# Kernel tuning notes

Hardware: AMD Instinct MI355X
Metric: run time of the kernel (lower is better)

## Reference

```python
import jax, jax.numpy as jnp
import numpy as np

B, N, C = 16, 2048, 256  # dim=256, hidden_dim=2*dim -> v,gate each width C
LN_EPS = 1e-5


def setup_inputs() -> dict:
    key = jax.random.key(0)
    ks = jax.random.split(key, 6)
    std = 0.02
    return {
        "x": jax.random.normal(ks[0], (B, N, C), dtype=jnp.float32),
        "H": 64,
        "W": 32,
        "ln_w": jnp.ones((C,), jnp.float32),
        "ln_b": jnp.zeros((C,), jnp.float32),
        "w_hidden": jax.random.normal(ks[1], (C, 2 * C), jnp.float32) * std,
        "b_hidden": jnp.zeros((2 * C,), jnp.float32),
        "w_kv": jax.random.normal(ks[2], (C, C), jnp.float32) * std,  # qkv_bias=False
        "gamma": jnp.ones((2, C), jnp.float32),   # torch.ones(2, dim)
        "beta": jnp.zeros((2, C), jnp.float32),   # torch.zeros(2, dim)
        "w_proj": jax.random.normal(ks[3], (C, C), jnp.float32) * std,
        "b_proj": jnp.zeros((C,), jnp.float32),
    }


def reference(x, H, W, ln_w, ln_b, w_hidden, b_hidden, w_kv, gamma, beta, w_proj, b_proj):
    # H, W are unused by the original forward (pos conv is dead code).
    b, n, c = x.shape
    # LayerNorm
    mu = jnp.mean(x, axis=-1, keepdims=True)
    var = jnp.mean(jnp.square(x - mu), axis=-1, keepdims=True)
    normed = (x - mu) * jax.lax.rsqrt(var + LN_EPS) * ln_w + ln_b
    # to_hidden: Linear + SiLU, then chunk into v, gate (each width c)
    h = jax.nn.silu(normed @ w_hidden + b_hidden)
    v, gate = h[..., :c], h[..., c:]
    # kv projection, then offset-scale into q, k
    Z = normed @ w_kv                                  # (b, n, c)
    QK = Z[..., None, :] * gamma + beta                # (b, n, 2, c)
    q, k = QK[..., 0, :], QK[..., 1, :]
    # relu^2 quadratic attention (no softmax)
    attn = jnp.einsum('bid,bjd->bij', q, k) / n        # (b, n, n)
    A = jnp.square(jax.nn.relu(attn))
    V = jnp.einsum('bij,bjd->bid', A, v)               # (b, n, c)
    # SiLU gating, output projection, residual
    out = (V * gate) @ w_proj + b_proj
    return out + x
```

## Files before the change

kernel.cpp:

```cpp
#include <hip/hip_runtime.h>

#define BN 32768
#define NB 16
#define NN 2048
#define CC 256
#define JT 64
#define NTILES (NN / JT)

using short8  = __attribute__((ext_vector_type(8))) short;
using floatx4 = __attribute__((ext_vector_type(4))) float;

__device__ __forceinline__ unsigned short f2bf(float f) {
  unsigned u = __builtin_bit_cast(unsigned, f);
  u += 0x7fffu + ((u >> 16) & 1u);
  return (unsigned short)(u >> 16);
}
__device__ __forceinline__ float bf2f(unsigned short h) {
  unsigned u = ((unsigned)h) << 16;
  return __builtin_bit_cast(float, u);
}
__device__ __forceinline__ unsigned pk4fp8(float a, float b, float c, float d) {
  unsigned u = __builtin_amdgcn_cvt_pk_fp8_f32(c, d, 0, true);
  return __builtin_amdgcn_cvt_pk_fp8_f32(a, b, (int)u, false);
}
__device__ __forceinline__ long lo64(uint4 v) {
  uint2 t; t.x = v.x; t.y = v.y; return __builtin_bit_cast(long, t);
}
__device__ __forceinline__ long hi64(uint4 v) {
  uint2 t; t.x = v.z; t.y = v.w; return __builtin_bit_cast(long, t);
}
__device__ __forceinline__ void gll16(const void* g, void* l) {
  __builtin_amdgcn_global_load_lds(
      (const __attribute__((address_space(1))) void*)g,
      (__attribute__((address_space(3))) void*)l, 16, 0, 0);
}

__global__ __launch_bounds__(256) void ln_kernel(
    const float* __restrict__ x, const float* __restrict__ lw,
    const float* __restrict__ lb, unsigned short* __restrict__ normed) {
  int row  = blockIdx.x * 4 + (threadIdx.x >> 6);
  int lane = threadIdx.x & 63;
  float4 v = ((const float4*)(x + (size_t)row * CC))[lane];
  float s  = v.x + v.y + v.z + v.w;
  float s2 = v.x * v.x + v.y * v.y + v.z * v.z + v.w * v.w;
#pragma unroll
  for (int off = 32; off; off >>= 1) {
    s  += __shfl_xor(s, off);
    s2 += __shfl_xor(s2, off);
  }
  float mu = s * (1.0f / CC);
  float rs = rsqrtf(s2 * (1.0f / CC) - mu * mu + 1e-5f);
  float4 w = ((const float4*)lw)[lane];
  float4 b = ((const float4*)lb)[lane];
  ushort4 o;
  o.x = f2bf((v.x - mu) * rs * w.x + b.x);
  o.y = f2bf((v.y - mu) * rs * w.y + b.y);
  o.z = f2bf((v.z - mu) * rs * w.z + b.z);
  o.w = f2bf((v.w - mu) * rs * w.w + b.w);
  ((ushort4*)(normed + (size_t)row * CC))[lane] = o;
}

__global__ __launch_bounds__(256) void wconv_kernel(
    const float* __restrict__ wh, const float* __restrict__ wkv,
    const float* __restrict__ wp,
    unsigned short* __restrict__ wTh, unsigned short* __restrict__ wTkv,
    unsigned short* __restrict__ wTp) {
  __shared__ float T[64][65];
  int bid = blockIdx.x;
  const float* src; unsigned short* dst; int N, kt, nt;
  if (bid < 32)      { src = wh;  dst = wTh;  N = 512; kt = bid >> 3;        nt = bid & 7; }
  else if (bid < 48) { src = wkv; dst = wTkv; N = 256; kt = (bid - 32) >> 2; nt = (bid - 32) & 3; }
  else               { src = wp;  dst = wTp;  N = 256; kt = (bid - 48) >> 2; nt = (bid - 48) & 3; }
  int k0 = kt * 64, n0 = nt * 64;
  int t = threadIdx.x;
  int r = t >> 2, c0 = (t & 3) * 16;
#pragma unroll
  for (int e = 0; e < 4; ++e)
    *(float4*)(&T[r][c0 + e * 4]) =
        *(const float4*)(src + (size_t)(k0 + r) * N + n0 + c0 + e * 4);
  __syncthreads();
#pragma unroll
  for (int e = 0; e < 16; ++e)
    dst[(size_t)(n0 + r) * 256 + k0 + c0 + e] = f2bf(T[c0 + e][r]);
}

__global__ __launch_bounds__(256) void gemm_v(
    const unsigned short* __restrict__ A, const unsigned short* __restrict__ BT,
    const float* __restrict__ bias, unsigned char* __restrict__ vB) {
  __shared__ unsigned char img[16384];
  int wave = threadIdx.x >> 6, lane = threadIdx.x & 63;
  int m = lane & 15, g4 = lane >> 4, kb = g4 * 8;
  int mb = blockIdx.x * 128;
  int nq = blockIdx.y * 128;
  int m0 = mb + (wave & 1) * 64;
  int n0 = nq + (wave >> 1) * 64;
  floatx4 acc[4][4] = {};
#pragma unroll
  for (int ks = 0; ks < 8; ++ks) {
    short8 af[4], bf[4];
#pragma unroll
    for (int i = 0; i < 4; ++i)
      af[i] = *(const short8*)(A + (size_t)(m0 + i * 16 + m) * CC + ks * 32 + kb);
#pragma unroll
    for (int j = 0; j < 4; ++j)
      bf[j] = *(const short8*)(BT + (size_t)(n0 + j * 16 + m) * CC + ks * 32 + kb);
#pragma unroll
    for (int i = 0; i < 4; ++i)
#pragma unroll
      for (int j = 0; j < 4; ++j)
        acc[i][j] = __builtin_amdgcn_mfma_f32_16x16x32_bf16(af[i], bf[j], acc[i][j], 0, 0, 0);
  }
  const int sw = (m >> 1) & 3;
  const int jtl = (wave & 1);
  const int jp4 = (g4 & 1) * 4;
  const int g4h = g4 >> 1;
#pragma unroll
  for (int j = 0; j < 4; ++j) {
    int col = n0 + j * 16 + m;
    int cl = col - nq;
    float bv = bias[col];
#pragma unroll
    for (int i = 0; i < 4; ++i) {
      int g4a = ((i * 2 + g4h) & 3) ^ sw;
      int h8 = ((i >> 1) & 1) * 8;
      float h, s0, s1, s2, s3;
      h = acc[i][j][0] + bv; s0 = h / (1.0f + __expf(-h));
      h = acc[i][j][1] + bv; s1 = h / (1.0f + __expf(-h));
      h = acc[i][j][2] + bv; s2 = h / (1.0f + __expf(-h));
      h = acc[i][j][3] + bv; s3 = h / (1.0f + __expf(-h));
      *(unsigned*)(img + jtl * 8192 + cl * 64 + g4a * 16 + h8 + jp4) =
          pk4fp8(s0, s1, s2, s3);
    }
  }
  __syncthreads();
  const size_t tb = ((size_t)(mb >> 11) * 32 + ((mb & 2047) >> 6)) * 16384;
#pragma unroll
  for (int it = 0; it < 4; ++it) {
    int o = it * 4096 + threadIdx.x * 16;
    int jl = o >> 13, rem = o & 8191;
    *(uint4*)(vB + tb + (size_t)jl * 16384 + (size_t)nq * 64 + rem) =
        *(const uint4*)(img + o);
  }
}

__global__ __launch_bounds__(256) void gemm_gate(
    const unsigned short* __restrict__ A, const unsigned short* __restrict__ BT,
    const float* __restrict__ bias, unsigned short* __restrict__ gout) {
  int wave = threadIdx.x >> 6, lane = threadIdx.x & 63;
  int m = lane & 15, g4 = lane >> 4, kb = g4 * 8;
  int m0 = blockIdx.x * 128 + (wave & 1) * 64;
  int n0 = 256 + blockIdx.y * 128 + (wave >> 1) * 64;
  floatx4 acc[4][4] = {};
#pragma unroll
  for (int ks = 0; ks < 8; ++ks) {
    short8 af[4], bf[4];
#pragma unroll
    for (int i = 0; i < 4; ++i)
      af[i] = *(const short8*)(A + (size_t)(m0 + i * 16 + m) * CC + ks * 32 + kb);
#pragma unroll
    for (int j = 0; j < 4; ++j)
      bf[j] = *(const short8*)(BT + (size_t)(n0 + j * 16 + m) * CC + ks * 32 + kb);
#pragma unroll
    for (int i = 0; i < 4; ++i)
#pragma unroll
      for (int j = 0; j < 4; ++j)
        acc[i][j] = __builtin_amdgcn_mfma_f32_16x16x32_bf16(af[i], bf[j], acc[i][j], 0, 0, 0);
  }
#pragma unroll
  for (int j = 0; j < 4; ++j) {
    int col = n0 + j * 16 + m;
    float bv = bias[col];
#pragma unroll
    for (int i = 0; i < 4; ++i)
#pragma unroll
      for (int r = 0; r < 4; ++r) {
        int row = m0 + i * 16 + g4 * 4 + r;
        float hh = acc[i][j][r] + bv;
        float sv = hh / (1.0f + __expf(-hh));
        gout[(size_t)row * CC + col - 256] = f2bf(sv);
      }
  }
}

__global__ __launch_bounds__(256) void gemm_kv(
    const unsigned short* __restrict__ A, const unsigned short* __restrict__ BT,
    const float* __restrict__ gamma, const float* __restrict__ beta,
    unsigned char* __restrict__ qout, unsigned char* __restrict__ kout) {
  __shared__ unsigned char kvimg[32768];
  int wave = threadIdx.x >> 6, lane = threadIdx.x & 63;
  int m = lane & 15, g4 = lane >> 4, kb = g4 * 8;
  int m0 = blockIdx.x * 128 + (wave & 1) * 64;
  int n0 = blockIdx.y * 128 + (wave >> 1) * 64;
  floatx4 acc[4][4] = {};
#pragma unroll
  for (int ks = 0; ks < 8; ++ks) {
    short8 af[4], bf[4];
#pragma unroll
    for (int i = 0; i < 4; ++i)
      af[i] = *(const short8*)(A + (size_t)(m0 + i * 16 + m) * CC + ks * 32 + kb);
#pragma unroll
    for (int j = 0; j < 4; ++j)
      bf[j] = *(const short8*)(BT + (size_t)(n0 + j * 16 + m) * CC + ks * 32 + kb);
#pragma unroll
    for (int i = 0; i < 4; ++i)
#pragma unroll
      for (int j = 0; j < 4; ++j)
        acc[i][j] = __builtin_amdgcn_mfma_f32_16x16x32_bf16(bf[j], af[i], acc[i][j], 0, 0, 0);
  }
  const int sw = (m >> 1) & 3;
  unsigned char* qi = kvimg;
  unsigned char* ki = kvimg + 16384;
  const int jbw = (wave & 1) * 4;
  const int ksl = (wave >> 1);
#pragma unroll
  for (int j = 0; j < 4; ++j) {
    int c4 = n0 + j * 16 + g4 * 4;
    float4 g0 = *(const float4*)(gamma + c4);
    float4 b0 = *(const float4*)(beta + c4);
    float4 g1 = *(const float4*)(gamma + CC + c4);
    float4 b1 = *(const float4*)(beta + CC + c4);
    int slot = ((c4 >> 3) & 3) ^ sw;
    int sub = slot * 16 + ((c4 >> 5) & 1) * 8 + (c4 & 7);
    int lbase = ksl * 1024 + m * 64 + sub;
#pragma unroll
    for (int i = 0; i < 4; ++i) {
      int off = (jbw + i) * 2048 + lbase;
      floatx4 z = acc[i][j];
      *(unsigned*)(qi + off) = pk4fp8(z[0] * g0.x + b0.x, z[1] * g0.y + b0.y,
                                      z[2] * g0.z + b0.z, z[3] * g0.w + b0.w);
      *(unsigned*)(ki + off) = pk4fp8(z[0] * g1.x + b1.x, z[1] * g1.y + b1.y,
                                      z[2] * g1.z + b1.z, z[3] * g1.w + b1.w);
    }
  }
  __syncthreads();
  const int mb = blockIdx.x * 128;
  const int jg0 = (mb & 2047) >> 4;
  const int kg0 = blockIdx.y * 2;
  const size_t gbase = ((size_t)(mb >> 11) * 128 + jg0) * 4096;
#pragma unroll
  for (int it = 0; it < 4; ++it) {
    int o = it * 4096 + threadIdx.x * 16;
    int jbl = o >> 11, rem = o & 2047;
    int ks2l = rem >> 10, r2 = rem & 1023;
    size_t gaddr = gbase + (size_t)jbl * 4096 + (size_t)(kg0 + ks2l) * 1024 + r2;
    *(uint4*)(kout + gaddr) = *(const uint4*)(ki + o);
    int n15 = (r2 >> 6) & 15;
    int slot = (r2 >> 4) & 3;
    int os = (o & ~48) | (((slot ^ ((n15 >> 1) & 3)) & 3) << 4);
    *(uint4*)(qout + gaddr) = *(const uint4*)(qi + os);
  }
}

__global__ __launch_bounds__(256, 2) void attn_kernel(
    const unsigned char* __restrict__ qB, const unsigned char* __restrict__ kB,
    const unsigned char* __restrict__ vB, const unsigned short* __restrict__ gg,
    unsigned short* __restrict__ og) {
  __shared__ unsigned char Kl[2][16384];
  __shared__ unsigned char Vl[2][16384];
  const int tid = threadIdx.x;
  const int wave = tid >> 6, lane = tid & 63;
  const int m = lane & 15, g4 = lane >> 4;
  const int id = blockIdx.x;
  const int b = id & 15, bx = id >> 4;
  const int i0 = bx * 64;
  const unsigned char* kimg = kB + (size_t)b * 524288;
  const unsigned char* vimg = vB + (size_t)b * 524288;

  const int iblk = bx * 4 + wave;
  uint4 qf[4];
#pragma unroll
  for (int ks2 = 0; ks2 < 4; ++ks2)
    qf[ks2] = *(const uint4*)(qB + ((size_t)(b * 128 + iblk) * 4 + ks2) * 1024 + m * 64 + g4 * 16);

  floatx4 acc[16] = {};
  const int alo = (m + ((g4 & 1) << 5)) << 2;
  const int ahi = alo + 64;
  const int gsw = (g4 ^ ((m >> 1) & 3)) * 16;

  auto stage = [&](int buf, int t) {
    const unsigned char* kt = kimg + (size_t)t * 16384;
    const unsigned char* vt = vimg + (size_t)t * 16384;
#pragma unroll
    for (int it = 0; it < 4; ++it) {
      int o = (it * 256 + tid) * 16;
      gll16(kt + o, &Kl[buf][o]);
      gll16(vt + o, &Vl[buf][o]);
    }
  };

  stage(0, 0);
  for (int t = 0; t < NTILES; ++t) {
    const int cur = t & 1;
    __syncthreads();
    if (t + 1 < NTILES) stage(cur ^ 1, t + 1);
    floatx4 sacc[4] = {};
#pragma unroll
    for (int ks2 = 0; ks2 < 4; ++ks2) {
#pragma unroll
      for (int jf = 0; jf < 4; ++jf) {
        uint4 kf = *(const uint4*)(&Kl[cur][(jf * 4 + ks2) * 1024 + m * 64 + gsw]);
        sacc[jf] = __builtin_amdgcn_mfma_f32_16x16x32_fp8_fp8(
            lo64(kf), lo64(qf[ks2]), sacc[jf], 0, 0, 0);
        sacc[jf] = __builtin_amdgcn_mfma_f32_16x16x32_fp8_fp8(
            hi64(kf), hi64(qf[ks2]), sacc[jf], 0, 0, 0);
      }
    }
    unsigned pk[4];
#pragma unroll
    for (int jf = 0; jf < 4; ++jf) {
      float p0 = fmaxf(sacc[jf][0], 0.0f) * 0.0625f;
      float p1 = fmaxf(sacc[jf][1], 0.0f) * 0.0625f;
      float p2 = fmaxf(sacc[jf][2], 0.0f) * 0.0625f;
      float p3 = fmaxf(sacc[jf][3], 0.0f) * 0.0625f;
      pk[jf] = pk4fp8(p0 * p0, p1 * p1, p2 * p2, p3 * p3);
    }
    long ap[2];
#pragma unroll
    for (int kk = 0; kk < 2; ++kk) {
      int A0 = __builtin_amdgcn_ds_bpermute(alo, (int)pk[2 * kk]);
      int B0 = __builtin_amdgcn_ds_bpermute(alo, (int)pk[2 * kk + 1]);
      int C0 = __builtin_amdgcn_ds_bpermute(ahi, (int)pk[2 * kk]);
      int D0 = __builtin_amdgcn_ds_bpermute(ahi, (int)pk[2 * kk + 1]);
      unsigned lo = (g4 & 2) ? (unsigned)B0 : (unsigned)A0;
      unsigned hi = (g4 & 2) ? (unsigned)D0 : (unsigned)C0;
      ap[kk] = (long)(((unsigned long long)hi << 32) | lo);
    }
#pragma unroll
    for (int cf = 0; cf < 16; ++cf) {
      uint4 vfr = *(const uint4*)(&Vl[cur][cf * 1024 + m * 64 + gsw]);
      acc[cf] = __builtin_amdgcn_mfma_f32_16x16x32_fp8_fp8(ap[0], lo64(vfr), acc[cf], 0, 0, 0);
      acc[cf] = __builtin_amdgcn_mfma_f32_16x16x32_fp8_fp8(ap[1], hi64(vfr), acc[cf], 0, 0, 0);
    }
  }
  const float sc = 1.0f / 16384.0f;
  const size_t bo = (size_t)b * NN * CC;
#pragma unroll
  for (int cf = 0; cf < 16; ++cf)
#pragma unroll
    for (int r = 0; r < 4; ++r) {
      int row = i0 + wave * 16 + g4 * 4 + r;
      int col = cf * 16 + m;
      size_t off = bo + (size_t)row * CC + col;
      og[off] = f2bf(acc[cf][r] * sc * bf2f(gg[off]));
    }
}

__global__ __launch_bounds__(256) void gemm_proj(
    const unsigned short* __restrict__ A, const unsigned short* __restrict__ BT,
    const float* __restrict__ bias, const float* __restrict__ xres,
    float* __restrict__ out) {
  int wave = threadIdx.x >> 6, lane = threadIdx.x & 63;
  int m = lane & 15, g4 = lane >> 4, kb = g4 * 8;
  int m0 = blockIdx.x * 128 + (wave & 1) * 64;
  int n0 = blockIdx.y * 128 + (wave >> 1) * 64;
  floatx4 acc[4][4] = {};
#pragma unroll
  for (int ks = 0; ks < 8; ++ks) {
    short8 af[4], bf[4];
#pragma unroll
    for (int i = 0; i < 4; ++i)
      af[i] = *(const short8*)(A + (size_t)(m0 + i * 16 + m) * CC + ks * 32 + kb);
#pragma unroll
    for (int j = 0; j < 4; ++j)
      bf[j] = *(const short8*)(BT + (size_t)(n0 + j * 16 + m) * CC + ks * 32 + kb);
#pragma unroll
    for (int i = 0; i < 4; ++i)
#pragma unroll
      for (int j = 0; j < 4; ++j)
        acc[i][j] = __builtin_amdgcn_mfma_f32_16x16x32_bf16(af[i], bf[j], acc[i][j], 0, 0, 0);
  }
#pragma unroll
  for (int j = 0; j < 4; ++j) {
    int col = n0 + j * 16 + m;
    float bv = bias[col];
#pragma unroll
    for (int i = 0; i < 4; ++i)
#pragma unroll
      for (int r = 0; r < 4; ++r) {
        int row = m0 + i * 16 + g4 * 4 + r;
        size_t rr = (size_t)row * CC;
        out[rr + col] = acc[i][j][r] + bv + xres[rr + col];
      }
  }
}

extern "C" void kernel_launch(void* const* d_in, const int* in_sizes, int n_in,
                              void* d_out, int out_size, void* d_ws, size_t ws_size,
                              hipStream_t stream) {
  const float* x        = (const float*)d_in[0];
  const float* ln_w     = (const float*)d_in[3];
  const float* ln_b     = (const float*)d_in[4];
  const float* w_hidden = (const float*)d_in[5];
  const float* b_hidden = (const float*)d_in[6];
  const float* w_kv     = (const float*)d_in[7];
  const float* gamma    = (const float*)d_in[8];
  const float* beta     = (const float*)d_in[9];
  const float* w_proj   = (const float*)d_in[10];
  const float* b_proj   = (const float*)d_in[11];
  float* out = (float*)d_out;
  char* ws = (char*)d_ws;

  const size_t SZ = (size_t)BN * CC * 2;
  const size_t HZ = SZ / 2;
  unsigned short* slot0 = (unsigned short*)(ws);
  unsigned short* gbuf  = (unsigned short*)(ws + SZ);
  unsigned char*  qB    = (unsigned char*)(ws + 2 * SZ);
  unsigned char*  kB    = (unsigned char*)(ws + 2 * SZ + HZ);
  unsigned char*  vB    = (unsigned char*)(ws + 2 * SZ + 2 * HZ);
  unsigned short* wTh   = (unsigned short*)(ws + 2 * SZ + 3 * HZ);
  unsigned short* wTkv  = (unsigned short*)(ws + 2 * SZ + 3 * HZ + 512 * 256 * 2);
  unsigned short* wTp   = (unsigned short*)(ws + 2 * SZ + 3 * HZ + 512 * 256 * 2 + 256 * 256 * 2);

  wconv_kernel<<<64, 256, 0, stream>>>(w_hidden, w_kv, w_proj, wTh, wTkv, wTp);
  ln_kernel<<<BN / 4, 256, 0, stream>>>(x, ln_w, ln_b, slot0);
  gemm_kv<<<dim3(BN / 128, 2), 256, 0, stream>>>(slot0, wTkv, gamma, beta, qB, kB);
  gemm_v<<<dim3(BN / 128, 2), 256, 0, stream>>>(slot0, wTh, b_hidden, vB);
  gemm_gate<<<dim3(BN / 128, 2), 256, 0, stream>>>(slot0, wTh, b_hidden, gbuf);
  attn_kernel<<<512, 256, 0, stream>>>(qB, kB, vB, gbuf, slot0);
  gemm_proj<<<dim3(BN / 128, 2), 256, 0, stream>>>(slot0, wTp, b_proj, x, out);
}
```

Baseline: 165.3 us.

## Fuse LayerNorm and the v, gate and kv projections into one producer kernel

Replaces the LayerNorm kernel and the three separate projection GEMMs with one kernel. Each 64-row block normalises its rows into an XOR-swizzled LDS tile and reuses that tile for the v, gate and q/k GEMMs. This removes three kernel launches and the bf16 normed round trip through global memory, and avoids re-reading the normed activations three times. The cost is a smaller M tile per block, so each block rereads the full weight matrices, and the q/k outputs are now written with scattered 4-byte stores instead of staged 16-byte stores.

```diff
diff --git a/kernel.cpp b/kernel.cpp
--- a/kernel.cpp
+++ b/kernel.cpp
@@ -34,30 +34,8 @@
       (const __attribute__((address_space(1))) void*)g,
       (__attribute__((address_space(3))) void*)l, 16, 0, 0);
 }
-
-__global__ __launch_bounds__(256) void ln_kernel(
-    const float* __restrict__ x, const float* __restrict__ lw,
-    const float* __restrict__ lb, unsigned short* __restrict__ normed) {
-  int row  = blockIdx.x * 4 + (threadIdx.x >> 6);
-  int lane = threadIdx.x & 63;
-  float4 v = ((const float4*)(x + (size_t)row * CC))[lane];
-  float s  = v.x + v.y + v.z + v.w;
-  float s2 = v.x * v.x + v.y * v.y + v.z * v.z + v.w * v.w;
-#pragma unroll
-  for (int off = 32; off; off >>= 1) {
-    s  += __shfl_xor(s, off);
-    s2 += __shfl_xor(s2, off);
-  }
-  float mu = s * (1.0f / CC);
-  float rs = rsqrtf(s2 * (1.0f / CC) - mu * mu + 1e-5f);
-  float4 w = ((const float4*)lw)[lane];
-  float4 b = ((const float4*)lb)[lane];
-  ushort4 o;
-  o.x = f2bf((v.x - mu) * rs * w.x + b.x);
-  o.y = f2bf((v.y - mu) * rs * w.y + b.y);
-  o.z = f2bf((v.z - mu) * rs * w.z + b.z);
-  o.w = f2bf((v.w - mu) * rs * w.w + b.w);
-  ((ushort4*)(normed + (size_t)row * CC))[lane] = o;
+__device__ __forceinline__ float silu(float h) {
+  return h / (1.0f + __expf(-h));
 }
 
 __global__ __launch_bounds__(256) void wconv_kernel(
@@ -84,170 +62,172 @@
     dst[(size_t)(n0 + r) * 256 + k0 + c0 + e] = f2bf(T[c0 + e][r]);
 }
 
-__global__ __launch_bounds__(256) void gemm_v(
-    const unsigned short* __restrict__ A, const unsigned short* __restrict__ BT,
-    const float* __restrict__ bias, unsigned char* __restrict__ vB) {
+__global__ __launch_bounds__(256) void producer_kernel(
+    const float* __restrict__ x, const float* __restrict__ lw,
+    const float* __restrict__ lb,
+    const unsigned short* __restrict__ wTh, const float* __restrict__ bh,
+    const unsigned short* __restrict__ wTkv,
+    const float* __restrict__ gamma, const float* __restrict__ beta,
+    unsigned char* __restrict__ vB, unsigned short* __restrict__ gout,
+    unsigned char* __restrict__ qout, unsigned char* __restrict__ kout) {
+  __shared__ unsigned short Al[64 * 256];
   __shared__ unsigned char img[16384];
-  int wave = threadIdx.x >> 6, lane = threadIdx.x & 63;
-  int m = lane & 15, g4 = lane >> 4, kb = g4 * 8;
-  int mb = blockIdx.x * 128;
-  int nq = blockIdx.y * 128;
-  int m0 = mb + (wave & 1) * 64;
-  int n0 = nq + (wave >> 1) * 64;
-  floatx4 acc[4][4] = {};
-#pragma unroll
-  for (int ks = 0; ks < 8; ++ks) {
-    short8 af[4], bf[4];
-#pragma unroll
-    for (int i = 0; i < 4; ++i)
-      af[i] = *(const short8*)(A + (size_t)(m0 + i * 16 + m) * CC + ks * 32 + kb);
-#pragma unroll
-    for (int j = 0; j < 4; ++j)
-      bf[j] = *(const short8*)(BT + (size_t)(n0 + j * 16 + m) * CC + ks * 32 + kb);
-#pragma unroll
-    for (int i = 0; i < 4; ++i)
+  const int t = threadIdx.x;
+  const int mb = blockIdx.x * 64;
+  {
+    int r = t >> 2, q = t & 3;
+    const float4* xp = (const float4*)(x + (size_t)(mb + r) * CC + q * 64);
+    float4 xv[16];
+#pragma unroll
+    for (int f = 0; f < 16; ++f) xv[f] = xp[f];
+    float s = 0.0f, s2 = 0.0f;
+#pragma unroll
+    for (int f = 0; f < 16; ++f) {
+      s  += xv[f].x + xv[f].y + xv[f].z + xv[f].w;
+      s2 += xv[f].x * xv[f].x + xv[f].y * xv[f].y
+          + xv[f].z * xv[f].z + xv[f].w * xv[f].w;
+    }
+    s  += __shfl_xor(s, 1);  s  += __shfl_xor(s, 2);
+    s2 += __shfl_xor(s2, 1); s2 += __shfl_xor(s2, 2);
+    float mu = s * (1.0f / CC);
+    float rs = rsqrtf(s2 * (1.0f / CC) - mu * mu + 1e-5f);
+    const float4* lwp = (const float4*)(lw + q * 64);
+    const float4* lbp = (const float4*)(lb + q * 64);
+#pragma unroll
+    for (int f = 0; f < 16; ++f) {
+      float4 w = lwp[f], b = lbp[f];
+      ushort4 o;
+      o.x = f2bf((xv[f].x - mu) * rs * w.x + b.x);
+      o.y = f2bf((xv[f].y - mu) * rs * w.y + b.y);
+      o.z = f2bf((xv[f].z - mu) * rs * w.z + b.z);
+      o.w = f2bf((xv[f].w - mu) * rs * w.w + b.w);
+      int c16 = q * 8 + (f >> 1);
+      *(ushort4*)((char*)Al + r * 512 + ((c16 ^ (r & 7)) * 16) + (f & 1) * 8) = o;
+    }
+  }
+  __syncthreads();
+  const int wave = t >> 6, lane = t & 63;
+  const int m = lane & 15, g4 = lane >> 4;
+  const int sw = (m >> 1) & 3;
+  const int phys_base = g4;
+  {
+    floatx4 acc[4][4] = {};
+#pragma unroll
+    for (int ks = 0; ks < 8; ++ks) {
+      short8 af[4], bf[4];
+#pragma unroll
+      for (int i = 0; i < 4; ++i)
+        af[i] = *(const short8*)((const char*)Al + (i * 16 + m) * 512 +
+                                 (((ks * 4 + phys_base) ^ (m & 7)) * 16));
 #pragma unroll
       for (int j = 0; j < 4; ++j)
-        acc[i][j] = __builtin_amdgcn_mfma_f32_16x16x32_bf16(af[i], bf[j], acc[i][j], 0, 0, 0);
-  }
-  const int sw = (m >> 1) & 3;
-  const int jtl = (wave & 1);
-  const int jp4 = (g4 & 1) * 4;
-  const int g4h = g4 >> 1;
-#pragma unroll
-  for (int j = 0; j < 4; ++j) {
-    int col = n0 + j * 16 + m;
-    int cl = col - nq;
-    float bv = bias[col];
-#pragma unroll
-    for (int i = 0; i < 4; ++i) {
-      int g4a = ((i * 2 + g4h) & 3) ^ sw;
-      int h8 = ((i >> 1) & 1) * 8;
-      float h, s0, s1, s2, s3;
-      h = acc[i][j][0] + bv; s0 = h / (1.0f + __expf(-h));
-      h = acc[i][j][1] + bv; s1 = h / (1.0f + __expf(-h));
-      h = acc[i][j][2] + bv; s2 = h / (1.0f + __expf(-h));
-      h = acc[i][j][3] + bv; s3 = h / (1.0f + __expf(-h));
-      *(unsigned*)(img + jtl * 8192 + cl * 64 + g4a * 16 + h8 + jp4) =
-          pk4fp8(s0, s1, s2, s3);
+        bf[j] = *(const short8*)(wTh + (size_t)(wave * 64 + j * 16 + m) * 256 + ks * 32 + g4 * 8);
+#pragma unroll
+      for (int i = 0; i < 4; ++i)
+#pragma unroll
+        for (int j = 0; j < 4; ++j)
+          acc[i][j] = __builtin_amdgcn_mfma_f32_16x16x32_bf16(af[i], bf[j], acc[i][j], 0, 0, 0);
+    }
+    const int jp4 = (g4 & 1) * 4;
+    const int g4h = g4 >> 1;
+#pragma unroll
+    for (int j = 0; j < 4; ++j) {
+      int col = wave * 64 + j * 16 + m;
+      float bv = bh[col];
+      int swc = (m >> 1) & 3;
+#pragma unroll
+      for (int i = 0; i < 4; ++i) {
+        int g4a = ((i * 2 + g4h) & 3) ^ swc;
+        int h8 = ((i >> 1) & 1) * 8;
+        float s0 = silu(acc[i][j][0] + bv);
+        float s1 = silu(acc[i][j][1] + bv);
+        float s2 = silu(acc[i][j][2] + bv);
+        float s3 = silu(acc[i][j][3] + bv);
+        *(unsigned*)(img + col * 64 + g4a * 16 + h8 + jp4) = pk4fp8(s0, s1, s2, s3);
+      }
+    }
+  }
+  {
+    floatx4 acc[4][4] = {};
+#pragma unroll
+    for (int ks = 0; ks < 8; ++ks) {
+      short8 af[4], bf[4];
+#pragma unroll
+      for (int i = 0; i < 4; ++i)
+        af[i] = *(const short8*)((const char*)Al + (i * 16 + m) * 512 +
+                                 (((ks * 4 + phys_base) ^ (m & 7)) * 16));
+#pragma unroll
+      for (int j = 0; j < 4; ++j)
+        bf[j] = *(const short8*)(wTh + (size_t)(256 + wave * 64 + j * 16 + m) * 256 + ks * 32 + g4 * 8);
+#pragma unroll
+      for (int i = 0; i < 4; ++i)
+#pragma unroll
+        for (int j = 0; j < 4; ++j)
+          acc[i][j] = __builtin_amdgcn_mfma_f32_16x16x32_bf16(af[i], bf[j], acc[i][j], 0, 0, 0);
+    }
+#pragma unroll
+    for (int j = 0; j < 4; ++j) {
+      int colg = wave * 64 + j * 16 + m;
+      float bv = bh[256 + colg];
+#pragma unroll
+      for (int i = 0; i < 4; ++i)
+#pragma unroll
+        for (int r = 0; r < 4; ++r) {
+          int row = mb + i * 16 + g4 * 4 + r;
+          gout[(size_t)row * CC + colg] = f2bf(silu(acc[i][j][r] + bv));
+        }
+    }
+  }
+  {
+    floatx4 acc[4][4] = {};
+#pragma unroll
+    for (int ks = 0; ks < 8; ++ks) {
+      short8 af[4], bf[4];
+#pragma unroll
+      for (int i = 0; i < 4; ++i)
+        af[i] = *(const short8*)((const char*)Al + (i * 16 + m) * 512 +
+                                 (((ks * 4 + phys_base) ^ (m & 7)) * 16));
+#pragma unroll
+      for (int j = 0; j < 4; ++j)
+        bf[j] = *(const short8*)(wTkv + (size_t)(wave * 64 + j * 16 + m) * 256 + ks * 32 + g4 * 8);
+#pragma unroll
+      for (int i = 0; i < 4; ++i)
+#pragma unroll
+        for (int j = 0; j < 4; ++j)
+          acc[i][j] = __builtin_amdgcn_mfma_f32_16x16x32_bf16(bf[j], af[i], acc[i][j], 0, 0, 0);
+    }
+#pragma unroll
+    for (int j = 0; j < 4; ++j) {
+      int c4 = wave * 64 + j * 16 + g4 * 4;
+      float4 g0 = *(const float4*)(gamma + c4);
+      float4 b0 = *(const float4*)(beta + c4);
+      float4 g1 = *(const float4*)(gamma + CC + c4);
+      float4 b1 = *(const float4*)(beta + CC + c4);
+      int ks2 = c4 >> 6;
+      int hsub = ((c4 >> 5) & 1) * 8 + (c4 & 7);
+      int qsub = ((c4 >> 3) & 3) * 16 + hsub;
+      int ksub = ((((c4 >> 3) & 3) ^ sw)) * 16 + hsub;
+#pragma unroll
+      for (int i = 0; i < 4; ++i) {
+        int n = mb + i * 16 + m;
+        int bb = n >> 11, jj = n & 2047;
+        size_t base = (((size_t)bb * 128 + (jj >> 4)) * 4 + ks2) * 1024 + (size_t)m * 64;
+        floatx4 z = acc[i][j];
+        *(unsigned*)(qout + base + qsub) = pk4fp8(z[0] * g0.x + b0.x, z[1] * g0.y + b0.y,
+                                                  z[2] * g0.z + b0.z, z[3] * g0.w + b0.w);
+        *(unsigned*)(kout + base + ksub) = pk4fp8(z[0] * g1.x + b1.x, z[1] * g1.y + b1.y,
+                                                  z[2] * g1.z + b1.z, z[3] * g1.w + b1.w);
+      }
     }
   }
   __syncthreads();
-  const size_t tb = ((size_t)(mb >> 11) * 32 + ((mb & 2047) >> 6)) * 16384;
-#pragma unroll
-  for (int it = 0; it < 4; ++it) {
-    int o = it * 4096 + threadIdx.x * 16;
-    int jl = o >> 13, rem = o & 8191;
-    *(uint4*)(vB + tb + (size_t)jl * 16384 + (size_t)nq * 64 + rem) =
-        *(const uint4*)(img + o);
-  }
-}
-
-__global__ __launch_bounds__(256) void gemm_gate(
-    const unsigned short* __restrict__ A, const unsigned short* __restrict__ BT,
-    const float* __restrict__ bias, unsigned short* __restrict__ gout) {
-  int wave = threadIdx.x >> 6, lane = threadIdx.x & 63;
-  int m = lane & 15, g4 = lane >> 4, kb = g4 * 8;
-  int m0 = blockIdx.x * 128 + (wave & 1) * 64;
-  int n0 = 256 + blockIdx.y * 128 + (wave >> 1) * 64;
-  floatx4 acc[4][4] = {};
-#pragma unroll
-  for (int ks = 0; ks < 8; ++ks) {
-    short8 af[4], bf[4];
-#pragma unroll
-    for (int i = 0; i < 4; ++i)
-      af[i] = *(const short8*)(A + (size_t)(m0 + i * 16 + m) * CC + ks * 32 + kb);
-#pragma unroll
-    for (int j = 0; j < 4; ++j)
-      bf[j] = *(const short8*)(BT + (size_t)(n0 + j * 16 + m) * CC + ks * 32 + kb);
-#pragma unroll
-    for (int i = 0; i < 4; ++i)
-#pragma unroll
-      for (int j = 0; j < 4; ++j)
-        acc[i][j] = __builtin_amdgcn_mfma_f32_16x16x32_bf16(af[i], bf[j], acc[i][j], 0, 0, 0);
-  }
-#pragma unroll
-  for (int j = 0; j < 4; ++j) {
-    int col = n0 + j * 16 + m;
-    float bv = bias[col];
-#pragma unroll
-    for (int i = 0; i < 4; ++i)
-#pragma unroll
-      for (int r = 0; r < 4; ++r) {
-        int row = m0 + i * 16 + g4 * 4 + r;
-        float hh = acc[i][j][r] + bv;
-        float sv = hh / (1.0f + __expf(-hh));
-        gout[(size_t)row * CC + col - 256] = f2bf(sv);
-      }
-  }
-}
-
-__global__ __launch_bounds__(256) void gemm_kv(
-    const unsigned short* __restrict__ A, const unsigned short* __restrict__ BT,
-    const float* __restrict__ gamma, const float* __restrict__ beta,
-    unsigned char* __restrict__ qout, unsigned char* __restrict__ kout) {
-  __shared__ unsigned char kvimg[32768];
-  int wave = threadIdx.x >> 6, lane = threadIdx.x & 63;
-  int m = lane & 15, g4 = lane >> 4, kb = g4 * 8;
-  int m0 = blockIdx.x * 128 + (wave & 1) * 64;
-  int n0 = blockIdx.y * 128 + (wave >> 1) * 64;
-  floatx4 acc[4][4] = {};
-#pragma unroll
-  for (int ks = 0; ks < 8; ++ks) {
-    short8 af[4], bf[4];
-#pragma unroll
-    for (int i = 0; i < 4; ++i)
-      af[i] = *(const short8*)(A + (size_t)(m0 + i * 16 + m) * CC + ks * 32 + kb);
-#pragma unroll
-    for (int j = 0; j < 4; ++j)
-      bf[j] = *(const short8*)(BT + (size_t)(n0 + j * 16 + m) * CC + ks * 32 + kb);
-#pragma unroll
-    for (int i = 0; i < 4; ++i)
-#pragma unroll
-      for (int j = 0; j < 4; ++j)
-        acc[i][j] = __builtin_amdgcn_mfma_f32_16x16x32_bf16(bf[j], af[i], acc[i][j], 0, 0, 0);
-  }
-  const int sw = (m >> 1) & 3;
-  unsigned char* qi = kvimg;
-  unsigned char* ki = kvimg + 16384;
-  const int jbw = (wave & 1) * 4;
-  const int ksl = (wave >> 1);
-#pragma unroll
-  for (int j = 0; j < 4; ++j) {
-    int c4 = n0 + j * 16 + g4 * 4;
-    float4 g0 = *(const float4*)(gamma + c4);
-    float4 b0 = *(const float4*)(beta + c4);
-    float4 g1 = *(const float4*)(gamma + CC + c4);
-    float4 b1 = *(const float4*)(beta + CC + c4);
-    int slot = ((c4 >> 3) & 3) ^ sw;
-    int sub = slot * 16 + ((c4 >> 5) & 1) * 8 + (c4 & 7);
-    int lbase = ksl * 1024 + m * 64 + sub;
-#pragma unroll
-    for (int i = 0; i < 4; ++i) {
-      int off = (jbw + i) * 2048 + lbase;
-      floatx4 z = acc[i][j];
-      *(unsigned*)(qi + off) = pk4fp8(z[0] * g0.x + b0.x, z[1] * g0.y + b0.y,
-                                      z[2] * g0.z + b0.z, z[3] * g0.w + b0.w);
-      *(unsigned*)(ki + off) = pk4fp8(z[0] * g1.x + b1.x, z[1] * g1.y + b1.y,
-                                      z[2] * g1.z + b1.z, z[3] * g1.w + b1.w);
-    }
-  }
-  __syncthreads();
-  const int mb = blockIdx.x * 128;
-  const int jg0 = (mb & 2047) >> 4;
-  const int kg0 = blockIdx.y * 2;
-  const size_t gbase = ((size_t)(mb >> 11) * 128 + jg0) * 4096;
-#pragma unroll
-  for (int it = 0; it < 4; ++it) {
-    int o = it * 4096 + threadIdx.x * 16;
-    int jbl = o >> 11, rem = o & 2047;
-    int ks2l = rem >> 10, r2 = rem & 1023;
-    size_t gaddr = gbase + (size_t)jbl * 4096 + (size_t)(kg0 + ks2l) * 1024 + r2;
-    *(uint4*)(kout + gaddr) = *(const uint4*)(ki + o);
-    int n15 = (r2 >> 6) & 15;
-    int slot = (r2 >> 4) & 3;
-    int os = (o & ~48) | (((slot ^ ((n15 >> 1) & 3)) & 3) << 4);
-    *(uint4*)(qout + gaddr) = *(const uint4*)(qi + os);
+  {
+    const size_t tb = ((size_t)(mb >> 11) * 32 + ((mb & 2047) >> 6)) * 16384;
+#pragma unroll
+    for (int it = 0; it < 4; ++it) {
+      int o = it * 4096 + t * 16;
+      *(uint4*)(vB + tb + o) = *(const uint4*)(img + o);
+    }
   }
 }
 
@@ -412,10 +392,8 @@
   unsigned short* wTp   = (unsigned short*)(ws + 2 * SZ + 3 * HZ + 512 * 256 * 2 + 256 * 256 * 2);
 
   wconv_kernel<<<64, 256, 0, stream>>>(w_hidden, w_kv, w_proj, wTh, wTkv, wTp);
-  ln_kernel<<<BN / 4, 256, 0, stream>>>(x, ln_w, ln_b, slot0);
-  gemm_kv<<<dim3(BN / 128, 2), 256, 0, stream>>>(slot0, wTkv, gamma, beta, qB, kB);
-  gemm_v<<<dim3(BN / 128, 2), 256, 0, stream>>>(slot0, wTh, b_hidden, vB);
-  gemm_gate<<<dim3(BN / 128, 2), 256, 0, stream>>>(slot0, wTh, b_hidden, gbuf);
+  producer_kernel<<<BN / 64, 256, 0, stream>>>(
+      x, ln_w, ln_b, wTh, b_hidden, wTkv, gamma, beta, vB, gbuf, qB, kB);
   attn_kernel<<<512, 256, 0, stream>>>(qB, kB, vB, gbuf, slot0);
   gemm_proj<<<dim3(BN / 128, 2), 256, 0, stream>>>(slot0, wTp, b_proj, x, out);
 }
```

After: 150.7 us. -8.8%, faster.
